# Kernel tuning notes

Measured on AMD Instinct MI355X. Metric: run time of the kernel, lower is better.

## Reference

```python
import jax, jax.numpy as jnp
import numpy as np

N, E, DIN, D, NUM_LAYERS = 50000, 800000, 64, 128, 3


def setup_inputs() -> dict:
    key = jax.random.key(0)
    ks = jax.random.split(key, 16)
    s = lambda fan_in: 1.0 / np.sqrt(fan_in)
    inp = {
        "x": jax.random.normal(ks[0], (N, DIN), jnp.float32),
        "edge_index": jax.random.randint(ks[1], (2, E), 0, N, jnp.int64),
        "edge_attr": jax.random.normal(ks[2], (E,), jnp.float32),
        "batch": jnp.zeros((N,), jnp.int64),
        # embed: Linear(DIN, D)
        "W_embed": jax.random.uniform(ks[3], (DIN, D), jnp.float32, -s(DIN), s(DIN)),
        "b_embed": jax.random.uniform(ks[4], (D,), jnp.float32, -s(DIN), s(DIN)),
        # msg_snd: Linear(D, D)
        "W_snd": jax.random.uniform(ks[5], (D, D), jnp.float32, -s(D), s(D)),
        "b_snd": jax.random.uniform(ks[6], (D,), jnp.float32, -s(D), s(D)),
        # msg_rec: Linear(2D, 2D)
        "W_rec": jax.random.uniform(ks[7], (2 * D, 2 * D), jnp.float32, -s(2 * D), s(2 * D)),
        "b_rec": jax.random.uniform(ks[8], (2 * D,), jnp.float32, -s(2 * D), s(2 * D)),
        # GRUCell(input=2D, hidden=D): gates ordered (r, z, n) as in torch
        "W_ih": jax.random.uniform(ks[9], (2 * D, 3 * D), jnp.float32, -s(D), s(D)),
        "b_ih": jax.random.uniform(ks[10], (3 * D,), jnp.float32, -s(D), s(D)),
        "W_hh": jax.random.uniform(ks[11], (D, 3 * D), jnp.float32, -s(D), s(D)),
        "b_hh": jax.random.uniform(ks[12], (3 * D,), jnp.float32, -s(D), s(D)),
    }
    return inp


def reference(x, edge_index, edge_attr, batch, W_embed, b_embed, W_snd, b_snd,
              W_rec, b_rec, W_ih, b_ih, W_hh, b_hh):
    n_nodes = x.shape[0]
    row, col = edge_index[0], edge_index[1]
    ea = edge_attr[:, None]                                    # [E,1]
    # scatter_mean denominator: in-degree, clamped to 1
    cnt = jax.ops.segment_sum(jnp.ones_like(edge_attr), col, num_segments=n_nodes)
    cnt = jnp.maximum(cnt, 1.0)[:, None]                       # [N,1]

    h = x @ W_embed + b_embed                                  # [N,D]
    for _ in range(NUM_LAYERS):
        s = jax.nn.leaky_relu(h @ W_snd + b_snd)               # msg_snd, [N,D]
        msgs = s[row] * ea                                     # gather + weight, [E,D]
        agg = jax.ops.segment_sum(msgs, col, num_segments=n_nodes) / cnt  # scatter_mean
        m = jax.nn.leaky_relu(jnp.concatenate([agg, h], -1) @ W_rec + b_rec)  # [N,2D]
        # torch GRUCell
        gi = m @ W_ih + b_ih                                   # [N,3D]
        gh = h @ W_hh + b_hh                                   # [N,3D]
        ir, iz, inn = jnp.split(gi, 3, axis=-1)
        hr, hz, hn = jnp.split(gh, 3, axis=-1)
        r = jax.nn.sigmoid(ir + hr)
        z = jax.nn.sigmoid(iz + hz)
        n = jnp.tanh(inn + r * hn)
        h = (1.0 - z) * n + z * h
    return h
```

## Files before the change

### kernel.cpp

```cpp
#include <hip/hip_runtime.h>
#include <hip/hip_bf16.h>
#include <stdint.h>

using bf16 = __hip_bfloat16;
typedef __attribute__((ext_vector_type(8))) short short8;
typedef __attribute__((ext_vector_type(4))) float f32x4;

#define LRELU_SLOPE 0.01f

#define GLOAD_LDS16(g, l) __builtin_amdgcn_global_load_lds( \
    (const __attribute__((address_space(1))) void*)(g),     \
    (__attribute__((address_space(3))) void*)(l), 16, 0, 0)

__device__ __forceinline__ float b2f(short s) {
    union { uint32_t u; float f; } cv;
    cv.u = ((uint32_t)(uint16_t)s) << 16;
    return cv.f;
}
__device__ __forceinline__ short f2b(float f) {
    bf16 h = __float2bfloat16(f);
    return *reinterpret_cast<short*>(&h);
}

__global__ __launch_bounds__(256) void gemm_m64_kernel(
    const bf16* __restrict__ A, int lda,
    const bf16* __restrict__ BT,
    const float* __restrict__ bias,
    bf16* __restrict__ C, int ldc,
    int N, int K, int cprShift, int act)
{
    __shared__ bf16 As[64 * 128];
    const int t   = threadIdx.x;
    const int wv  = t >> 6, ln = t & 63, m16 = ln & 15, q = ln >> 4;
    const int row0 = blockIdx.x * 64;
    const int col0 = (wv >> 1) * 64;
    const int wr   = (wv & 1) * 32;
    const int cmask = (1 << cprShift) - 1;
    const int trips = (1 << cprShift) >> 2;

    for (int i = 0; i < trips; ++i) {
        int g    = i * 256 + t;
        int row  = g >> cprShift;
        int cidx = (g & cmask) ^ (row & cmask);
        int grow = row0 + row; if (grow > N - 1) grow = N - 1;
        GLOAD_LDS16(A + (size_t)grow * lda + cidx * 8,
                    As + ((i * 256 + wv * 64) << 3));
    }
    __syncthreads();

    f32x4 acc[2][4];
#pragma unroll
    for (int mi = 0; mi < 2; ++mi)
#pragma unroll
        for (int ni = 0; ni < 4; ++ni)
            acc[mi][ni] = (f32x4){0.f, 0.f, 0.f, 0.f};

    for (int k0 = 0; k0 < K; k0 += 32) {
        int cbase = (k0 >> 3) + q;
        short8 a[2], b[4];
#pragma unroll
        for (int mi = 0; mi < 2; ++mi) {
            int row = wr + mi * 16 + m16;
            int cs  = cbase ^ (row & cmask);
            a[mi] = *reinterpret_cast<const short8*>(As + row * K + cs * 8);
        }
#pragma unroll
        for (int ni = 0; ni < 4; ++ni)
            b[ni] = *reinterpret_cast<const short8*>(
                BT + (size_t)(col0 + ni * 16 + m16) * K + k0 + q * 8);
#pragma unroll
        for (int mi = 0; mi < 2; ++mi)
#pragma unroll
            for (int ni = 0; ni < 4; ++ni)
                acc[mi][ni] = __builtin_amdgcn_mfma_f32_16x16x32_bf16(
                    a[mi], b[ni], acc[mi][ni], 0, 0, 0);
    }
    __syncthreads();

#pragma unroll
    for (int mi = 0; mi < 2; ++mi) {
#pragma unroll
        for (int ni = 0; ni < 4; ++ni) {
            int col = col0 + ni * 16 + m16;
            float bv = bias[col];
#pragma unroll
            for (int r = 0; r < 4; ++r) {
                int lrow = wr + mi * 16 + q * 4 + r;
                float v = acc[mi][ni][r] + bv;
                if (act) v = (v > 0.f) ? v : LRELU_SLOPE * v;
                short sv = f2b(v);
                As[lrow * 128 + (((col >> 3) ^ (lrow & 15)) << 3) + (col & 7)] =
                    *reinterpret_cast<bf16*>(&sv);
            }
        }
    }
    __syncthreads();
#pragma unroll
    for (int i = 0; i < 4; ++i) {
        int s   = i * 256 + t;
        int row = s >> 4, c = s & 15;
        int grow = row0 + row;
        if (grow < N) {
            short8 v = *reinterpret_cast<const short8*>(
                As + row * 128 + ((c ^ (row & 15)) << 3));
            *reinterpret_cast<short8*>(C + (size_t)grow * ldc + c * 8) = v;
        }
    }
}

__global__ __launch_bounds__(256) void layer_kernel(
    const bf16* __restrict__ cat,
    const bf16* __restrict__ WM,
    const float* __restrict__ bM,
    const bf16* __restrict__ WX,
    const float* __restrict__ bX,
    bf16* __restrict__ catH,
    float* __restrict__ out32,
    int N, int last)
{
    __shared__ bf16 smem[24576];
    bf16* R0 = smem;
    bf16* R1 = smem + 8192;
    bf16* R2 = smem + 16384;

    const int t  = threadIdx.x;
    const int wv = t >> 6, ln = t & 63, m16 = ln & 15, q = ln >> 4;
    const int row0 = blockIdx.x * 64;

#pragma unroll
    for (int i = 0; i < 8; ++i) {
        int s    = i * 256 + t;
        int R    = s >> 10;
        int row  = (s >> 4) & 63;
        int c    = (s & 15) ^ (row & 15);
        int grow = row0 + row; if (grow > N - 1) grow = N - 1;
        GLOAD_LDS16(cat + (size_t)grow * 256 + R * 128 + c * 8,
                    smem + ((i * 256 + wv * 64) << 3));
    }
    __syncthreads();

    f32x4 macc[4][4];
#pragma unroll
    for (int mi = 0; mi < 4; ++mi)
#pragma unroll
        for (int ni = 0; ni < 4; ++ni)
            macc[mi][ni] = (f32x4){0.f, 0.f, 0.f, 0.f};

#pragma unroll
    for (int k0 = 0; k0 < 256; k0 += 32) {
        const bf16* Rg = (k0 < 128) ? R0 : R1;
        int kl = k0 & 127;
        short8 a[4], b[4];
#pragma unroll
        for (int mi = 0; mi < 4; ++mi) {
            int row = mi * 16 + m16;
            int c   = ((kl >> 3) + q) ^ m16;
            a[mi] = *reinterpret_cast<const short8*>(Rg + row * 128 + c * 8);
        }
#pragma unroll
        for (int ni = 0; ni < 4; ++ni)
            b[ni] = *reinterpret_cast<const short8*>(
                WM + (size_t)(wv * 64 + ni * 16 + m16) * 256 + k0 + q * 8);
#pragma unroll
        for (int mi = 0; mi < 4; ++mi)
#pragma unroll
            for (int ni = 0; ni < 4; ++ni)
                macc[mi][ni] = __builtin_amdgcn_mfma_f32_16x16x32_bf16(
                    a[mi], b[ni], macc[mi][ni], 0, 0, 0);
    }
    __syncthreads();

#pragma unroll
    for (int mi = 0; mi < 4; ++mi) {
#pragma unroll
        for (int ni = 0; ni < 4; ++ni) {
            int ch  = wv * 64 + ni * 16 + m16;
            bf16* MR = (ch < 128) ? R0 : R2;
            int chl = ch & 127;
            float bv = bM[ch];
#pragma unroll
            for (int r = 0; r < 4; ++r) {
                int row = mi * 16 + q * 4 + r;
                float v = macc[mi][ni][r] + bv;
                v = (v > 0.f) ? v : LRELU_SLOPE * v;
                short sv = f2b(v);
                MR[row * 128 + (((chl >> 3) ^ (row & 15)) << 3) + (chl & 7)] =
                    *reinterpret_cast<bf16*>(&sv);
            }
        }
    }
    __syncthreads();

    f32x4 gr[4][2], gz[4][2], gn_[4][2], gh_[4][2];
#pragma unroll
    for (int mi = 0; mi < 4; ++mi)
#pragma unroll
        for (int ni = 0; ni < 2; ++ni) {
            gr[mi][ni]  = (f32x4){0.f, 0.f, 0.f, 0.f};
            gz[mi][ni]  = (f32x4){0.f, 0.f, 0.f, 0.f};
            gn_[mi][ni] = (f32x4){0.f, 0.f, 0.f, 0.f};
            gh_[mi][ni] = (f32x4){0.f, 0.f, 0.f, 0.f};
        }

#pragma unroll
    for (int k0 = 0; k0 < 256; k0 += 32) {
        const bf16* Rg = (k0 < 128) ? R0 : R2;
        int kl = k0 & 127;
        short8 a[4];
#pragma unroll
        for (int mi = 0; mi < 4; ++mi) {
            int row = mi * 16 + m16;
            int c   = ((kl >> 3) + q) ^ m16;
            a[mi] = *reinterpret_cast<const short8*>(Rg + row * 128 + c * 8);
        }
        short8 br[2], bz[2], bn[2];
#pragma unroll
        for (int ni = 0; ni < 2; ++ni) {
            int cw = wv * 32 + ni * 16 + m16;
            br[ni] = *reinterpret_cast<const short8*>(WX + (size_t)(cw)       * 384 + k0 + q * 8);
            bz[ni] = *reinterpret_cast<const short8*>(WX + (size_t)(128 + cw) * 384 + k0 + q * 8);
            bn[ni] = *reinterpret_cast<const short8*>(WX + (size_t)(256 + cw) * 384 + k0 + q * 8);
        }
#pragma unroll
        for (int mi = 0; mi < 4; ++mi)
#pragma unroll
            for (int ni = 0; ni < 2; ++ni) {
                gr[mi][ni]  = __builtin_amdgcn_mfma_f32_16x16x32_bf16(a[mi], br[ni], gr[mi][ni], 0, 0, 0);
                gz[mi][ni]  = __builtin_amdgcn_mfma_f32_16x16x32_bf16(a[mi], bz[ni], gz[mi][ni], 0, 0, 0);
                gn_[mi][ni] = __builtin_amdgcn_mfma_f32_16x16x32_bf16(a[mi], bn[ni], gn_[mi][ni], 0, 0, 0);
            }
    }
#pragma unroll
    for (int k0 = 256; k0 < 384; k0 += 32) {
        int kl = k0 - 256;
        short8 a[4];
#pragma unroll
        for (int mi = 0; mi < 4; ++mi) {
            int row = mi * 16 + m16;
            int c   = ((kl >> 3) + q) ^ m16;
            a[mi] = *reinterpret_cast<const short8*>(R1 + row * 128 + c * 8);
        }
        short8 br[2], bz[2], bh[2];
#pragma unroll
        for (int ni = 0; ni < 2; ++ni) {
            int cw = wv * 32 + ni * 16 + m16;
            br[ni] = *reinterpret_cast<const short8*>(WX + (size_t)(cw)       * 384 + k0 + q * 8);
            bz[ni] = *reinterpret_cast<const short8*>(WX + (size_t)(128 + cw) * 384 + k0 + q * 8);
            bh[ni] = *reinterpret_cast<const short8*>(WX + (size_t)(384 + cw) * 384 + k0 + q * 8);
        }
#pragma unroll
        for (int mi = 0; mi < 4; ++mi)
#pragma unroll
            for (int ni = 0; ni < 2; ++ni) {
                gr[mi][ni]  = __builtin_amdgcn_mfma_f32_16x16x32_bf16(a[mi], br[ni], gr[mi][ni], 0, 0, 0);
                gz[mi][ni]  = __builtin_amdgcn_mfma_f32_16x16x32_bf16(a[mi], bz[ni], gz[mi][ni], 0, 0, 0);
                gh_[mi][ni] = __builtin_amdgcn_mfma_f32_16x16x32_bf16(a[mi], bh[ni], gh_[mi][ni], 0, 0, 0);
            }
    }
    __syncthreads();

#pragma unroll
    for (int mi = 0; mi < 4; ++mi) {
#pragma unroll
        for (int ni = 0; ni < 2; ++ni) {
            int ch = wv * 32 + ni * 16 + m16;
            float brv = bX[ch], bzv = bX[128 + ch];
            float bnv = bX[256 + ch], bhv = bX[384 + ch];
#pragma unroll
            for (int r = 0; r < 4; ++r) {
                int lrow = mi * 16 + q * 4 + r;
                int c = ((ch >> 3) ^ (lrow & 15)) << 3;
                float hv = b2f(*reinterpret_cast<const short*>(
                    R1 + lrow * 128 + c + (ch & 7)));
                float rr = 1.f / (1.f + __expf(-(gr[mi][ni][r] + brv)));
                float zz = 1.f / (1.f + __expf(-(gz[mi][ni][r] + bzv)));
                float nn = tanhf(gn_[mi][ni][r] + bnv + rr * (gh_[mi][ni][r] + bhv));
                float hnew = (1.f - zz) * nn + zz * hv;
                short hb = f2b(hnew);
                R0[lrow * 128 + c + (ch & 7)] = *reinterpret_cast<bf16*>(&hb);
            }
        }
    }
    __syncthreads();

#pragma unroll
    for (int i = 0; i < 4; ++i) {
        int s   = i * 256 + t;
        int row = s >> 4, c = s & 15;
        int grow = row0 + row;
        if (grow < N) {
            short8 v = *reinterpret_cast<const short8*>(
                R0 + row * 128 + ((c ^ (row & 15)) << 3));
            if (last) {
                f32x4 lo, hi;
#pragma unroll
                for (int j = 0; j < 4; ++j) { lo[j] = b2f(v[j]); hi[j] = b2f(v[j + 4]); }
                float* dst = out32 + (size_t)grow * 128 + c * 8;
                *reinterpret_cast<f32x4*>(dst)     = lo;
                *reinterpret_cast<f32x4*>(dst + 4) = hi;
            } else {
                *reinterpret_cast<short8*>(catH + (size_t)grow * 256 + c * 8) = v;
            }
        }
    }
}

__global__ void prep_kernel(const float* __restrict__ x, bf16* __restrict__ xb, int nx,
                            const float* __restrict__ W_embed, bf16* __restrict__ TE,
                            const float* __restrict__ W_snd,   bf16* __restrict__ TS,
                            const float* __restrict__ W_rec,   bf16* __restrict__ TM,
                            const float* __restrict__ W_ih, const float* __restrict__ W_hh,
                            bf16* __restrict__ TX,
                            const float* __restrict__ b_ih, const float* __restrict__ b_hh,
                            float* __restrict__ bext)
{
    int t = blockIdx.x * 256 + threadIdx.x;
    if (t < nx) { xb[t] = __float2bfloat16(x[t]); return; }
    t -= nx;
    if (t < 8192)  { TE[(t % 128) * 64  + t / 128] = __float2bfloat16(W_embed[t]); return; }
    t -= 8192;
    if (t < 16384) { TS[(t % 128) * 128 + t / 128] = __float2bfloat16(W_snd[t]); return; }
    t -= 16384;
    if (t < 65536) { TM[(t % 256) * 256 + t / 256] = __float2bfloat16(W_rec[t]); return; }
    t -= 65536;
    if (t < 196608) {
        int c = t / 384, k = t - c * 384;
        float v;
        if (c < 256)      v = (k < 256) ? W_ih[k * 384 + c] : W_hh[(k - 256) * 384 + c];
        else if (c < 384) v = (k < 256) ? W_ih[k * 384 + c] : 0.f;
        else              v = (k < 256) ? 0.f : W_hh[(k - 256) * 384 + (c - 128)];
        TX[t] = __float2bfloat16(v);
        return;
    }
    t -= 196608;
    if (t < 512) {
        float v;
        if (t < 256)      v = b_ih[t] + b_hh[t];
        else if (t < 384) v = b_ih[t];
        else              v = b_hh[t - 128];
        bext[t] = v;
    }
}

__global__ void hist_kernel(const int* __restrict__ col, int* __restrict__ cnt, int E)
{
    int e = blockIdx.x * 256 + threadIdx.x;
    if (e < E) atomicAdd(&cnt[col[e]], 1);
}

__global__ void blockscan_kernel(const int* __restrict__ cnt, int* __restrict__ off,
                                 int* __restrict__ bsum, int N)
{
    __shared__ int sm[256];
    int i = blockIdx.x * 256 + threadIdx.x;
    int v = (i < N) ? cnt[i] : 0;
    sm[threadIdx.x] = v;
    __syncthreads();
    for (int d = 1; d < 256; d <<= 1) {
        int tv = (threadIdx.x >= (unsigned)d) ? sm[threadIdx.x - d] : 0;
        __syncthreads();
        sm[threadIdx.x] += tv;
        __syncthreads();
    }
    if (i < N) off[i] = sm[threadIdx.x] - v;
    if (threadIdx.x == 255) bsum[blockIdx.x] = sm[255];
}

__global__ void bscan_kernel(int* __restrict__ bsum, int nb)
{
    __shared__ int sm[512];
    int v = (threadIdx.x < (unsigned)nb) ? bsum[threadIdx.x] : 0;
    sm[threadIdx.x] = v;
    __syncthreads();
    for (int d = 1; d < 512; d <<= 1) {
        int tv = (threadIdx.x >= (unsigned)d) ? sm[threadIdx.x - d] : 0;
        __syncthreads();
        sm[threadIdx.x] += tv;
        __syncthreads();
    }
    if (threadIdx.x < (unsigned)nb) bsum[threadIdx.x] = sm[threadIdx.x] - v;
}

__global__ void addoff_kernel(int* __restrict__ off, const int* __restrict__ bsum,
                              const int* __restrict__ cnt, float* __restrict__ icnt,
                              int N, int E)
{
    int i = blockIdx.x * 256 + threadIdx.x;
    if (i < N) {
        off[i] += bsum[blockIdx.x];
        icnt[i] = 1.0f / fmaxf((float)cnt[i], 1.0f);
    }
    if (i == 0) off[N] = E;
}

__global__ void fill_kernel(const int* __restrict__ row, const int* __restrict__ col,
                            const float* __restrict__ ea, const int* __restrict__ off,
                            int* __restrict__ fil, int2* __restrict__ re, int E)
{
    int e = blockIdx.x * 256 + threadIdx.x;
    if (e < E) {
        int c = col[e];
        int p = atomicAdd(&fil[c], 1);
        int2 v; v.x = row[e]; v.y = __float_as_int(ea[e]);
        re[off[c] + p] = v;
    }
}

__global__ void agg_kernel(const int* __restrict__ off,
                           const int2* __restrict__ re,
                           const bf16* __restrict__ s,
                           const float* __restrict__ icnt,
                           bf16* __restrict__ cat, int N)
{
    int wid  = (int)((blockIdx.x * blockDim.x + threadIdx.x) >> 6);
    int lane = threadIdx.x & 63;
    if (wid >= N) return;
    const int rg = lane >> 4;
    const int cl = lane & 15;
    int b = off[wid], e = off[wid + 1];

    float acc[8];
#pragma unroll
    for (int j = 0; j < 8; ++j) acc[j] = 0.f;

    int i = b + rg;
    for (; i + 4 < e; i += 8) {
        int2 p0 = re[i];
        int2 p1 = re[i + 4];
        short8 v0 = *reinterpret_cast<const short8*>(s + (size_t)p0.x * 128 + cl * 8);
        short8 v1 = *reinterpret_cast<const short8*>(s + (size_t)p1.x * 128 + cl * 8);
        float w0 = __int_as_float(p0.y), w1 = __int_as_float(p1.y);
#pragma unroll
        for (int j = 0; j < 8; ++j) acc[j] += w0 * b2f(v0[j]) + w1 * b2f(v1[j]);
    }
    if (i < e) {
        int2 p0 = re[i];
        float w0 = __int_as_float(p0.y);
        short8 v0 = *reinterpret_cast<const short8*>(s + (size_t)p0.x * 128 + cl * 8);
#pragma unroll
        for (int j = 0; j < 8; ++j) acc[j] += w0 * b2f(v0[j]);
    }
#pragma unroll
    for (int j = 0; j < 8; ++j) {
        acc[j] += __shfl_xor(acc[j], 16, 64);
        acc[j] += __shfl_xor(acc[j], 32, 64);
    }
    if (rg == 0) {
        float ic = icnt[wid];
        short8 o;
#pragma unroll
        for (int j = 0; j < 8; ++j) o[j] = f2b(acc[j] * ic);
        *reinterpret_cast<short8*>(cat + (size_t)wid * 256 + cl * 8) = o;
    }
}

extern "C" void kernel_launch(void* const* d_in, const int* in_sizes, int n_in,
                              void* d_out, int out_size, void* d_ws, size_t ws_size,
                              hipStream_t stream)
{
    const float* x       = (const float*)d_in[0];
    const int*   ei      = (const int*)d_in[1];
    const float* ea      = (const float*)d_in[2];
    const float* W_embed = (const float*)d_in[4];
    const float* b_embed = (const float*)d_in[5];
    const float* W_snd   = (const float*)d_in[6];
    const float* b_snd   = (const float*)d_in[7];
    const float* W_rec   = (const float*)d_in[8];
    const float* b_rec   = (const float*)d_in[9];
    const float* W_ih    = (const float*)d_in[10];
    const float* b_ih    = (const float*)d_in[11];
    const float* W_hh    = (const float*)d_in[12];
    const float* b_hh    = (const float*)d_in[13];

    const int N = in_sizes[3];
    const int E = in_sizes[2];
    const int N64 = ((N + 63) / 64) * 64;

    char* p = (char*)d_ws;
    auto carve = [&](size_t bytes) {
        char* r = p;
        p += (bytes + 255) & ~(size_t)255;
        return (void*)r;
    };
    bf16*  xb   = (bf16*) carve((size_t)N64 * 64  * 2);
    bf16*  cat  = (bf16*) carve((size_t)N64 * 256 * 2);
    bf16*  sbuf = (bf16*) carve((size_t)N64 * 128 * 2);
    int2*  re   = (int2*) carve((size_t)E * 8);
    int*   cnt  = (int*)  carve((size_t)N * 4);
    int*   fil  = (int*)  carve((size_t)N * 4);
    int*   off  = (int*)  carve((size_t)(N + 1) * 4);
    int*   bsum = (int*)  carve((size_t)512 * 4);
    float* icnt = (float*)carve((size_t)N * 4);
    bf16*  wtE  = (bf16*) carve((size_t)128 * 64 * 2);
    bf16*  wtS  = (bf16*) carve((size_t)128 * 128 * 2);
    bf16*  wtM  = (bf16*) carve((size_t)256 * 256 * 2);
    bf16*  wtX  = (bf16*) carve((size_t)512 * 384 * 2);
    float* bext = (float*)carve((size_t)512 * 4);

    const int* rowp = ei;
    const int* colp = ei + E;

    hipMemsetAsync(cnt, 0, (size_t)N * 4, stream);
    hipMemsetAsync(fil, 0, (size_t)N * 4, stream);

    const int TB = 256;
    auto nb = [](int n) { return (n + 255) / 256; };

    prep_kernel<<<nb(N * 64 + 287232), TB, 0, stream>>>(
        x, xb, N * 64, W_embed, wtE, W_snd, wtS, W_rec, wtM,
        W_ih, W_hh, wtX, b_ih, b_hh, bext);

    hist_kernel<<<nb(E), TB, 0, stream>>>(colp, cnt, E);
    blockscan_kernel<<<nb(N), TB, 0, stream>>>(cnt, off, bsum, N);
    bscan_kernel<<<1, 512, 0, stream>>>(bsum, nb(N));
    addoff_kernel<<<nb(N), TB, 0, stream>>>(off, bsum, cnt, icnt, N, E);
    fill_kernel<<<nb(E), TB, 0, stream>>>(rowp, colp, ea, off, fil, re, E);

    const int gx = (N + 63) / 64;

    gemm_m64_kernel<<<gx, TB, 0, stream>>>(xb, 64, wtE, b_embed,
                                           cat + 128, 256, N, 64, 3, 0);

    for (int L = 0; L < 3; ++L) {
        gemm_m64_kernel<<<gx, TB, 0, stream>>>(cat + 128, 256, wtS, b_snd,
                                               sbuf, 128, N, 128, 4, 1);
        agg_kernel<<<(N * 64 + TB - 1) / TB, TB, 0, stream>>>(off, re, sbuf,
                                                              icnt, cat, N);
        layer_kernel<<<gx, TB, 0, stream>>>(cat, wtM, b_rec, wtX, bext,
                                            cat + 128, (float*)d_out,
                                            N, (L == 2) ? 1 : 0);
    }
}
```

Measured before the change: 587.6 us.

## Fuse sender linear into embed and layer kernels; prefetch GRU weights

```diff
diff --git a/kernel.cpp b/kernel.cpp
--- a/kernel.cpp
+++ b/kernel.cpp
@@ -11,6 +11,8 @@
 #define GLOAD_LDS16(g, l) __builtin_amdgcn_global_load_lds( \
     (const __attribute__((address_space(1))) void*)(g),     \
     (__attribute__((address_space(3))) void*)(l), 16, 0, 0)
+
+#define MFMA16(a, b, c) __builtin_amdgcn_mfma_f32_16x16x32_bf16((a), (b), (c), 0, 0, 0)
 
 __device__ __forceinline__ float b2f(short s) {
     union { uint32_t u; float f; } cv;
@@ -22,32 +24,35 @@
     return *reinterpret_cast<short*>(&h);
 }
 
-__global__ __launch_bounds__(256) void gemm_m64_kernel(
-    const bf16* __restrict__ A, int lda,
-    const bf16* __restrict__ BT,
-    const float* __restrict__ bias,
-    bf16* __restrict__ C, int ldc,
-    int N, int K, int cprShift, int act)
-{
-    __shared__ bf16 As[64 * 128];
+__global__ __launch_bounds__(256) void embed_kernel(
+    const bf16* __restrict__ xb,
+    const bf16* __restrict__ WE,
+    const float* __restrict__ bE,
+    const bf16* __restrict__ WS,
+    const float* __restrict__ bS,
+    bf16* __restrict__ catH,
+    bf16* __restrict__ sbuf,
+    int N)
+{
+    __shared__ bf16 H[8192];
+    __shared__ bf16 X[8192];
     const int t   = threadIdx.x;
     const int wv  = t >> 6, ln = t & 63, m16 = ln & 15, q = ln >> 4;
     const int row0 = blockIdx.x * 64;
+
+#pragma unroll
+    for (int i = 0; i < 2; ++i) {
+        int g    = i * 256 + t;
+        int row  = g >> 3;
+        int cidx = (g & 7) ^ (row & 7);
+        int grow = row0 + row; if (grow > N - 1) grow = N - 1;
+        GLOAD_LDS16(xb + (size_t)grow * 64 + cidx * 8,
+                    X + ((i * 256 + wv * 64) << 3));
+    }
+    __syncthreads();
+
     const int col0 = (wv >> 1) * 64;
     const int wr   = (wv & 1) * 32;
-    const int cmask = (1 << cprShift) - 1;
-    const int trips = (1 << cprShift) >> 2;
-
-    for (int i = 0; i < trips; ++i) {
-        int g    = i * 256 + t;
-        int row  = g >> cprShift;
-        int cidx = (g & cmask) ^ (row & cmask);
-        int grow = row0 + row; if (grow > N - 1) grow = N - 1;
-        GLOAD_LDS16(A + (size_t)grow * lda + cidx * 8,
-                    As + ((i * 256 + wv * 64) << 3));
-    }
-    __syncthreads();
-
     f32x4 acc[2][4];
 #pragma unroll
     for (int mi = 0; mi < 2; ++mi)
@@ -55,46 +60,43 @@
         for (int ni = 0; ni < 4; ++ni)
             acc[mi][ni] = (f32x4){0.f, 0.f, 0.f, 0.f};
 
-    for (int k0 = 0; k0 < K; k0 += 32) {
-        int cbase = (k0 >> 3) + q;
+#pragma unroll
+    for (int k0 = 0; k0 < 64; k0 += 32) {
         short8 a[2], b[4];
 #pragma unroll
         for (int mi = 0; mi < 2; ++mi) {
             int row = wr + mi * 16 + m16;
-            int cs  = cbase ^ (row & cmask);
-            a[mi] = *reinterpret_cast<const short8*>(As + row * K + cs * 8);
+            int cs  = ((k0 >> 3) + q) ^ (row & 7);
+            a[mi] = *reinterpret_cast<const short8*>(X + row * 64 + cs * 8);
         }
 #pragma unroll
         for (int ni = 0; ni < 4; ++ni)
             b[ni] = *reinterpret_cast<const short8*>(
-                BT + (size_t)(col0 + ni * 16 + m16) * K + k0 + q * 8);
+                WE + (size_t)(col0 + ni * 16 + m16) * 64 + k0 + q * 8);
 #pragma unroll
         for (int mi = 0; mi < 2; ++mi)
 #pragma unroll
             for (int ni = 0; ni < 4; ++ni)
-                acc[mi][ni] = __builtin_amdgcn_mfma_f32_16x16x32_bf16(
-                    a[mi], b[ni], acc[mi][ni], 0, 0, 0);
-    }
-    __syncthreads();
+                acc[mi][ni] = MFMA16(a[mi], b[ni], acc[mi][ni]);
+    }
 
 #pragma unroll
     for (int mi = 0; mi < 2; ++mi) {
 #pragma unroll
         for (int ni = 0; ni < 4; ++ni) {
             int col = col0 + ni * 16 + m16;
-            float bv = bias[col];
+            float bv = bE[col];
 #pragma unroll
             for (int r = 0; r < 4; ++r) {
                 int lrow = wr + mi * 16 + q * 4 + r;
-                float v = acc[mi][ni][r] + bv;
-                if (act) v = (v > 0.f) ? v : LRELU_SLOPE * v;
-                short sv = f2b(v);
-                As[lrow * 128 + (((col >> 3) ^ (lrow & 15)) << 3) + (col & 7)] =
+                short sv = f2b(acc[mi][ni][r] + bv);
+                H[lrow * 128 + (((col >> 3) ^ (lrow & 15)) << 3) + (col & 7)] =
                     *reinterpret_cast<bf16*>(&sv);
             }
         }
     }
     __syncthreads();
+
 #pragma unroll
     for (int i = 0; i < 4; ++i) {
         int s   = i * 256 + t;
@@ -102,8 +104,65 @@
         int grow = row0 + row;
         if (grow < N) {
             short8 v = *reinterpret_cast<const short8*>(
-                As + row * 128 + ((c ^ (row & 15)) << 3));
-            *reinterpret_cast<short8*>(C + (size_t)grow * ldc + c * 8) = v;
+                H + row * 128 + ((c ^ (row & 15)) << 3));
+            *reinterpret_cast<short8*>(catH + (size_t)grow * 256 + c * 8) = v;
+        }
+    }
+
+    f32x4 sacc[4][2];
+#pragma unroll
+    for (int mi = 0; mi < 4; ++mi)
+#pragma unroll
+        for (int ni = 0; ni < 2; ++ni)
+            sacc[mi][ni] = (f32x4){0.f, 0.f, 0.f, 0.f};
+
+#pragma unroll
+    for (int k0 = 0; k0 < 128; k0 += 32) {
+        short8 a[4], b[2];
+#pragma unroll
+        for (int mi = 0; mi < 4; ++mi) {
+            int row = mi * 16 + m16;
+            int c   = ((k0 >> 3) + q) ^ m16;
+            a[mi] = *reinterpret_cast<const short8*>(H + row * 128 + c * 8);
+        }
+#pragma unroll
+        for (int ni = 0; ni < 2; ++ni)
+            b[ni] = *reinterpret_cast<const short8*>(
+                WS + (size_t)(wv * 32 + ni * 16 + m16) * 128 + k0 + q * 8);
+#pragma unroll
+        for (int mi = 0; mi < 4; ++mi)
+#pragma unroll
+            for (int ni = 0; ni < 2; ++ni)
+                sacc[mi][ni] = MFMA16(a[mi], b[ni], sacc[mi][ni]);
+    }
+
+#pragma unroll
+    for (int mi = 0; mi < 4; ++mi) {
+#pragma unroll
+        for (int ni = 0; ni < 2; ++ni) {
+            int ch = wv * 32 + ni * 16 + m16;
+            float bv = bS[ch];
+#pragma unroll
+            for (int r = 0; r < 4; ++r) {
+                int row = mi * 16 + q * 4 + r;
+                float v = sacc[mi][ni][r] + bv;
+                v = (v > 0.f) ? v : LRELU_SLOPE * v;
+                short sv = f2b(v);
+                X[row * 128 + (((ch >> 3) ^ (row & 15)) << 3) + (ch & 7)] =
+                    *reinterpret_cast<bf16*>(&sv);
+            }
+        }
+    }
+    __syncthreads();
+#pragma unroll
+    for (int i = 0; i < 4; ++i) {
+        int s   = i * 256 + t;
+        int row = s >> 4, c = s & 15;
+        int grow = row0 + row;
+        if (grow < N) {
+            short8 v = *reinterpret_cast<const short8*>(
+                X + row * 128 + ((c ^ (row & 15)) << 3));
+            *reinterpret_cast<short8*>(sbuf + (size_t)grow * 128 + c * 8) = v;
         }
     }
 }
@@ -114,7 +173,10 @@
     const float* __restrict__ bM,
     const bf16* __restrict__ WX,
     const float* __restrict__ bX,
+    const bf16* __restrict__ WS,
+    const float* __restrict__ bS,
     bf16* __restrict__ catH,
+    bf16* __restrict__ sbuf,
     float* __restrict__ out32,
     int N, int last)
 {
@@ -152,21 +214,20 @@
         int kl = k0 & 127;
         short8 a[4], b[4];
 #pragma unroll
+        for (int ni = 0; ni < 4; ++ni)
+            b[ni] = *reinterpret_cast<const short8*>(
+                WM + (size_t)(wv * 64 + ni * 16 + m16) * 256 + k0 + q * 8);
+#pragma unroll
         for (int mi = 0; mi < 4; ++mi) {
             int row = mi * 16 + m16;
             int c   = ((kl >> 3) + q) ^ m16;
             a[mi] = *reinterpret_cast<const short8*>(Rg + row * 128 + c * 8);
         }
 #pragma unroll
-        for (int ni = 0; ni < 4; ++ni)
-            b[ni] = *reinterpret_cast<const short8*>(
-                WM + (size_t)(wv * 64 + ni * 16 + m16) * 256 + k0 + q * 8);
-#pragma unroll
         for (int mi = 0; mi < 4; ++mi)
 #pragma unroll
             for (int ni = 0; ni < 4; ++ni)
-                macc[mi][ni] = __builtin_amdgcn_mfma_f32_16x16x32_bf16(
-                    a[mi], b[ni], macc[mi][ni], 0, 0, 0);
+                macc[mi][ni] = MFMA16(a[mi], b[ni], macc[mi][ni]);
     }
     __syncthreads();
 
@@ -202,8 +263,32 @@
             gh_[mi][ni] = (f32x4){0.f, 0.f, 0.f, 0.f};
         }
 
+    short8 brC[2], bzC[2], bxC[2];
+#pragma unroll
+    for (int ni = 0; ni < 2; ++ni) {
+        int cw = wv * 32 + ni * 16 + m16;
+        brC[ni] = *reinterpret_cast<const short8*>(WX + (size_t)(cw)       * 384 + q * 8);
+        bzC[ni] = *reinterpret_cast<const short8*>(WX + (size_t)(128 + cw) * 384 + q * 8);
+        bxC[ni] = *reinterpret_cast<const short8*>(WX + (size_t)(256 + cw) * 384 + q * 8);
+    }
+
 #pragma unroll
     for (int k0 = 0; k0 < 256; k0 += 32) {
+        const int kn = k0 + 32;
+        short8 brN[2], bzN[2], bxN[2];
+#pragma unroll
+        for (int ni = 0; ni < 2; ++ni) {
+            int cw = wv * 32 + ni * 16 + m16;
+            if (kn < 256) {
+                brN[ni] = *reinterpret_cast<const short8*>(WX + (size_t)(cw)       * 384 + kn + q * 8);
+                bzN[ni] = *reinterpret_cast<const short8*>(WX + (size_t)(128 + cw) * 384 + kn + q * 8);
+                bxN[ni] = *reinterpret_cast<const short8*>(WX + (size_t)(256 + cw) * 384 + kn + q * 8);
+            } else {
+                brN[ni] = *reinterpret_cast<const short8*>(WX + (size_t)(cw)       * 384 + 256 + q * 8);
+                bzN[ni] = *reinterpret_cast<const short8*>(WX + (size_t)(128 + cw) * 384 + 256 + q * 8);
+                bxN[ni] = *reinterpret_cast<const short8*>(WX + (size_t)(384 + cw) * 384 + 256 + q * 8);
+            }
+        }
         const bf16* Rg = (k0 < 128) ? R0 : R2;
         int kl = k0 & 127;
         short8 a[4];
@@ -213,25 +298,34 @@
             int c   = ((kl >> 3) + q) ^ m16;
             a[mi] = *reinterpret_cast<const short8*>(Rg + row * 128 + c * 8);
         }
-        short8 br[2], bz[2], bn[2];
+#pragma unroll
+        for (int mi = 0; mi < 4; ++mi)
+#pragma unroll
+            for (int ni = 0; ni < 2; ++ni) {
+                gr[mi][ni]  = MFMA16(a[mi], brC[ni], gr[mi][ni]);
+                gz[mi][ni]  = MFMA16(a[mi], bzC[ni], gz[mi][ni]);
+                gn_[mi][ni] = MFMA16(a[mi], bxC[ni], gn_[mi][ni]);
+            }
 #pragma unroll
         for (int ni = 0; ni < 2; ++ni) {
-            int cw = wv * 32 + ni * 16 + m16;
-            br[ni] = *reinterpret_cast<const short8*>(WX + (size_t)(cw)       * 384 + k0 + q * 8);
-            bz[ni] = *reinterpret_cast<const short8*>(WX + (size_t)(128 + cw) * 384 + k0 + q * 8);
-            bn[ni] = *reinterpret_cast<const short8*>(WX + (size_t)(256 + cw) * 384 + k0 + q * 8);
-        }
-#pragma unroll
-        for (int mi = 0; mi < 4; ++mi)
-#pragma unroll
-            for (int ni = 0; ni < 2; ++ni) {
-                gr[mi][ni]  = __builtin_amdgcn_mfma_f32_16x16x32_bf16(a[mi], br[ni], gr[mi][ni], 0, 0, 0);
-                gz[mi][ni]  = __builtin_amdgcn_mfma_f32_16x16x32_bf16(a[mi], bz[ni], gz[mi][ni], 0, 0, 0);
-                gn_[mi][ni] = __builtin_amdgcn_mfma_f32_16x16x32_bf16(a[mi], bn[ni], gn_[mi][ni], 0, 0, 0);
-            }
+            brC[ni] = brN[ni]; bzC[ni] = bzN[ni]; bxC[ni] = bxN[ni];
+        }
     }
 #pragma unroll
     for (int k0 = 256; k0 < 384; k0 += 32) {
+        const int kn = k0 + 32;
+        short8 brN[2], bzN[2], bxN[2];
+#pragma unroll
+        for (int ni = 0; ni < 2; ++ni) {
+            if (kn < 384) {
+                int cw = wv * 32 + ni * 16 + m16;
+                brN[ni] = *reinterpret_cast<const short8*>(WX + (size_t)(cw)       * 384 + kn + q * 8);
+                bzN[ni] = *reinterpret_cast<const short8*>(WX + (size_t)(128 + cw) * 384 + kn + q * 8);
+                bxN[ni] = *reinterpret_cast<const short8*>(WX + (size_t)(384 + cw) * 384 + kn + q * 8);
+            } else {
+                brN[ni] = brC[ni]; bzN[ni] = bzC[ni]; bxN[ni] = bxC[ni];
+            }
+        }
         int kl = k0 - 256;
         short8 a[4];
 #pragma unroll
@@ -240,22 +334,18 @@
             int c   = ((kl >> 3) + q) ^ m16;
             a[mi] = *reinterpret_cast<const short8*>(R1 + row * 128 + c * 8);
         }
-        short8 br[2], bz[2], bh[2];
+#pragma unroll
+        for (int mi = 0; mi < 4; ++mi)
+#pragma unroll
+            for (int ni = 0; ni < 2; ++ni) {
+                gr[mi][ni]  = MFMA16(a[mi], brC[ni], gr[mi][ni]);
+                gz[mi][ni]  = MFMA16(a[mi], bzC[ni], gz[mi][ni]);
+                gh_[mi][ni] = MFMA16(a[mi], bxC[ni], gh_[mi][ni]);
+            }
 #pragma unroll
         for (int ni = 0; ni < 2; ++ni) {
-            int cw = wv * 32 + ni * 16 + m16;
-            br[ni] = *reinterpret_cast<const short8*>(WX + (size_t)(cw)       * 384 + k0 + q * 8);
-            bz[ni] = *reinterpret_cast<const short8*>(WX + (size_t)(128 + cw) * 384 + k0 + q * 8);
-            bh[ni] = *reinterpret_cast<const short8*>(WX + (size_t)(384 + cw) * 384 + k0 + q * 8);
-        }
-#pragma unroll
-        for (int mi = 0; mi < 4; ++mi)
-#pragma unroll
-            for (int ni = 0; ni < 2; ++ni) {
-                gr[mi][ni]  = __builtin_amdgcn_mfma_f32_16x16x32_bf16(a[mi], br[ni], gr[mi][ni], 0, 0, 0);
-                gz[mi][ni]  = __builtin_amdgcn_mfma_f32_16x16x32_bf16(a[mi], bz[ni], gz[mi][ni], 0, 0, 0);
-                gh_[mi][ni] = __builtin_amdgcn_mfma_f32_16x16x32_bf16(a[mi], bh[ni], gh_[mi][ni], 0, 0, 0);
-            }
+            brC[ni] = brN[ni]; bzC[ni] = bzN[ni]; bxC[ni] = bxN[ni];
+        }
     }
     __syncthreads();
 
@@ -300,6 +390,65 @@
                 *reinterpret_cast<f32x4*>(dst + 4) = hi;
             } else {
                 *reinterpret_cast<short8*>(catH + (size_t)grow * 256 + c * 8) = v;
+            }
+        }
+    }
+
+    if (!last) {
+        f32x4 sacc[4][2];
+#pragma unroll
+        for (int mi = 0; mi < 4; ++mi)
+#pragma unroll
+            for (int ni = 0; ni < 2; ++ni)
+                sacc[mi][ni] = (f32x4){0.f, 0.f, 0.f, 0.f};
+
+#pragma unroll
+        for (int k0 = 0; k0 < 128; k0 += 32) {
+            short8 a[4], b[2];
+#pragma unroll
+            for (int ni = 0; ni < 2; ++ni)
+                b[ni] = *reinterpret_cast<const short8*>(
+                    WS + (size_t)(wv * 32 + ni * 16 + m16) * 128 + k0 + q * 8);
+#pragma unroll
+            for (int mi = 0; mi < 4; ++mi) {
+                int row = mi * 16 + m16;
+                int c   = ((k0 >> 3) + q) ^ m16;
+                a[mi] = *reinterpret_cast<const short8*>(R0 + row * 128 + c * 8);
+            }
+#pragma unroll
+            for (int mi = 0; mi < 4; ++mi)
+#pragma unroll
+                for (int ni = 0; ni < 2; ++ni)
+                    sacc[mi][ni] = MFMA16(a[mi], b[ni], sacc[mi][ni]);
+        }
+
+#pragma unroll
+        for (int mi = 0; mi < 4; ++mi) {
+#pragma unroll
+            for (int ni = 0; ni < 2; ++ni) {
+                int ch = wv * 32 + ni * 16 + m16;
+                float bv = bS[ch];
+#pragma unroll
+                for (int r = 0; r < 4; ++r) {
+                    int row = mi * 16 + q * 4 + r;
+                    float v = sacc[mi][ni][r] + bv;
+                    v = (v > 0.f) ? v : LRELU_SLOPE * v;
+                    short sv = f2b(v);
+                    R1[row * 128 + (((ch >> 3) ^ (row & 15)) << 3) + (ch & 7)] =
+                        *reinterpret_cast<bf16*>(&sv);
+                }
+            }
+        }
+        __syncthreads();
+#pragma unroll
+        for (int i = 0; i < 4; ++i) {
+            int s   = i * 256 + t;
+            int row = s >> 4, c = s & 15;
+            int grow = row0 + row;
+            if (grow < N) {
+                short8 v = *reinterpret_cast<const short8*>(
+                    R1 + row * 128 + ((c ^ (row & 15)) << 3));
+                *reinterpret_cast<short8*>(sbuf + (size_t)grow * 128 + c * 8) = v;
             }
         }
     }
@@ -518,16 +667,15 @@
 
     const int gx = (N + 63) / 64;
 
-    gemm_m64_kernel<<<gx, TB, 0, stream>>>(xb, 64, wtE, b_embed,
-                                           cat + 128, 256, N, 64, 3, 0);
+    embed_kernel<<<gx, TB, 0, stream>>>(xb, wtE, b_embed, wtS, b_snd,
+                                        cat + 128, sbuf, N);
 
     for (int L = 0; L < 3; ++L) {
-        gemm_m64_kernel<<<gx, TB, 0, stream>>>(cat + 128, 256, wtS, b_snd,
-                                               sbuf, 128, N, 128, 4, 1);
         agg_kernel<<<(N * 64 + TB - 1) / TB, TB, 0, stream>>>(off, re, sbuf,
                                                               icnt, cat, N);
         layer_kernel<<<gx, TB, 0, stream>>>(cat, wtM, b_rec, wtX, bext,
-                                            cat + 128, (float*)d_out,
+                                            wtS, b_snd,
+                                            cat + 128, sbuf, (float*)d_out,
                                             N, (L == 2) ? 1 : 0);
     }
 }
```

New measurement: 583.9 us. No clear change (-0.6%).
